# Kernel optimization log

Measured on AMD Instinct MI355X. Metric: run time of the kernel, lower is better.

The kernel has to match this reference:

```python
import jax, jax.numpy as jnp
import numpy as np

N_SAMPLES = 2 ** 16  # 65536


def sparse_softmax(x, axis=-1):
    # forward: one-hot at argmax (normalize=True -> value 1.0)
    # backward: softmax gradient (straight-through)
    sm = jax.nn.softmax(x, axis=axis)
    hard = jax.nn.one_hot(jnp.argmax(sm, axis=axis), x.shape[axis], dtype=x.dtype)
    return sm + jax.lax.stop_gradient(hard - sm)


def upsample_with_holes(x, desired_size):
    # strided zero-insertion: out[..., ::step] = x
    step = desired_size // x.shape[-1]
    out = jnp.zeros(x.shape[:-1] + (desired_size,), dtype=x.dtype)
    return out.at[..., ::step].set(x)


def fft_convolve(a, b):
    # circular-safe convolution: pad both to 2n, multiply spectra, keep first n
    n = a.shape[-1]
    pad_a = [(0, 0)] * (a.ndim - 1) + [(0, n)]
    pad_b = [(0, 0)] * (b.ndim - 1) + [(0, n)]
    spec = jnp.fft.rfft(jnp.pad(a, pad_a), axis=-1) * jnp.fft.rfft(jnp.pad(b, pad_b), axis=-1)
    return jnp.fft.irfft(spec, axis=-1)[..., :n]


def setup_inputs() -> dict:
    key = jax.random.key(0)
    k1, k2 = jax.random.split(key)
    events = jax.random.normal(k1, (8, 32, N_SAMPLES), dtype=jnp.float32)
    # nn.Parameter uniform_(-1, 1)
    pos = jax.random.uniform(k2, (1, 32, 1024), dtype=jnp.float32, minval=-1.0, maxval=1.0)
    return {"events": events, "pos": pos}


def reference(events, pos):
    p = sparse_softmax(pos, axis=-1)                 # (1, 32, 1024) one-hot
    p = upsample_with_holes(p, N_SAMPLES)            # (1, 32, 65536) sparse diracs
    return fft_convolve(events, p)                   # (8, 32, 65536)
```

## Files before the change

kernel.cpp:

```cpp
#include <hip/hip_runtime.h>

#define N_SAMPLES 65536
#define POS_LEN   1024
#define STEP      64
#define NCH       32
#define NB        8
#define ROW4      (N_SAMPLES / 4)

__global__ void argmax_kernel(const float* __restrict__ pos, int* __restrict__ delay) {
    const int c    = blockIdx.x;
    const int lane = threadIdx.x;
    const float* row = pos + c * POS_LEN;

    float best = -__builtin_inff();
    int   bidx = POS_LEN;
    for (int k = lane; k < POS_LEN; k += 64) {
        float v = row[k];
        if (v > best) { best = v; bidx = k; }
    }
    for (int off = 32; off > 0; off >>= 1) {
        float ov = __shfl_down(best, off, 64);
        int   oi = __shfl_down(bidx, off, 64);
        if (ov > best || (ov == best && oi < bidx)) { best = ov; bidx = oi; }
    }
    if (lane == 0) delay[c] = bidx * STEP;
}

__global__ void shift_kernel(const float4* __restrict__ in, float4* __restrict__ out,
                             const int* __restrict__ delay) {
    __shared__ int sdelay4[NCH];
    if (threadIdx.x < NCH) sdelay4[threadIdx.x] = delay[threadIdx.x] >> 2;
    __syncthreads();

    const int total  = NB * NCH * ROW4;
    const int stride = gridDim.x * blockDim.x;
    for (int i = blockIdx.x * blockDim.x + threadIdx.x; i < total; i += stride) {
        const int t4 = i & (ROW4 - 1);
        const int c  = (i >> 14) & (NCH - 1);
        const int d4 = sdelay4[c];
        float4 v;
        if (t4 >= d4) {
            v = in[i - d4];
        } else {
            v = make_float4(0.f, 0.f, 0.f, 0.f);
        }
        out[i] = v;
    }
}

extern "C" void kernel_launch(void* const* d_in, const int* in_sizes, int n_in,
                              void* d_out, int out_size, void* d_ws, size_t ws_size,
                              hipStream_t stream) {
    const float* events = (const float*)d_in[0];
    const float* pos    = (const float*)d_in[1];
    float*       out    = (float*)d_out;
    int*         delay  = (int*)d_ws;

    argmax_kernel<<<NCH, 64, 0, stream>>>(pos, delay);

    shift_kernel<<<2048, 256, 0, stream>>>((const float4*)events, (float4*)out, delay);
}
```

Baseline: 119.6 us.

## Fuse argmax into shift kernel with per-row segment blocks and nontemporal I/O

Merges the argmax and shift kernels into one launch. Each block recomputes its channel's argmax with a 256-thread reduction and then copies one segment of a row with a fixed unrolled loop, using nontemporal loads and stores. This removes a kernel launch, the workspace round trip and the dependency between the two kernels. In exchange, each of the 2048 blocks redundantly reads 4 KB of pos and performs a block reduction with two syncs before streaming.

Measured after the change: 118.9 us. Within noise of the previous version (-0.6%).

```diff
diff --git a/kernel.cpp b/kernel.cpp
--- a/kernel.cpp
+++ b/kernel.cpp
@@ -6,45 +6,64 @@
 #define NCH       32
 #define NB        8
 #define ROW4      (N_SAMPLES / 4)
+#define SEGS      8
+#define SEG4      (ROW4 / SEGS)
 
-__global__ void argmax_kernel(const float* __restrict__ pos, int* __restrict__ delay) {
-    const int c    = blockIdx.x;
-    const int lane = threadIdx.x;
-    const float* row = pos + c * POS_LEN;
+typedef float f32x4 __attribute__((ext_vector_type(4)));
 
-    float best = -__builtin_inff();
-    int   bidx = POS_LEN;
-    for (int k = lane; k < POS_LEN; k += 64) {
-        float v = row[k];
-        if (v > best) { best = v; bidx = k; }
+__global__ __launch_bounds__(256) void dirac_shift(const float* __restrict__ pos,
+                                                   const f32x4* __restrict__ in,
+                                                   f32x4* __restrict__ out) {
+    const int g   = blockIdx.x;
+    const int row = g >> 3;
+    const int seg = g & (SEGS - 1);
+    const int c   = row & (NCH - 1);
+    const int tid = threadIdx.x;
+
+    __shared__ float swv[4];
+    __shared__ int   swi[4];
+    __shared__ int   sd4;
+
+    {
+        const f32x4 v = ((const f32x4*)(pos + c * POS_LEN))[tid];
+        float best = v[0];
+        int   bidx = tid * 4;
+        #pragma unroll
+        for (int j = 1; j < 4; ++j) {
+            if (v[j] > best) { best = v[j]; bidx = tid * 4 + j; }
+        }
+        #pragma unroll
+        for (int off = 32; off > 0; off >>= 1) {
+            float ov = __shfl_down(best, off, 64);
+            int   oi = __shfl_down(bidx, off, 64);
+            if (ov > best || (ov == best && oi < bidx)) { best = ov; bidx = oi; }
+        }
+        const int lane = tid & 63, wave = tid >> 6;
+        if (lane == 0) { swv[wave] = best; swi[wave] = bidx; }
     }
-    for (int off = 32; off > 0; off >>= 1) {
-        float ov = __shfl_down(best, off, 64);
-        int   oi = __shfl_down(bidx, off, 64);
-        if (ov > best || (ov == best && oi < bidx)) { best = ov; bidx = oi; }
+    __syncthreads();
+    if (tid == 0) {
+        float best = swv[0];
+        int   bidx = swi[0];
+        #pragma unroll
+        for (int w = 1; w < 4; ++w) {
+            if (swv[w] > best || (swv[w] == best && swi[w] < bidx)) { best = swv[w]; bidx = swi[w]; }
+        }
+        sd4 = bidx * (STEP / 4);
     }
-    if (lane == 0) delay[c] = bidx * STEP;
-}
-
-__global__ void shift_kernel(const float4* __restrict__ in, float4* __restrict__ out,
-                             const int* __restrict__ delay) {
-    __shared__ int sdelay4[NCH];
-    if (threadIdx.x < NCH) sdelay4[threadIdx.x] = delay[threadIdx.x] >> 2;
     __syncthreads();
 
-    const int total  = NB * NCH * ROW4;
-    const int stride = gridDim.x * blockDim.x;
-    for (int i = blockIdx.x * blockDim.x + threadIdx.x; i < total; i += stride) {
-        const int t4 = i & (ROW4 - 1);
-        const int c  = (i >> 14) & (NCH - 1);
-        const int d4 = sdelay4[c];
-        float4 v;
-        if (t4 >= d4) {
-            v = in[i - d4];
-        } else {
-            v = make_float4(0.f, 0.f, 0.f, 0.f);
-        }
-        out[i] = v;
+    const int d4 = sd4;
+    const f32x4* inrow  = in  + (size_t)row * ROW4;
+    f32x4*       outrow = out + (size_t)row * ROW4;
+    const int base = seg * SEG4;
+
+    #pragma unroll
+    for (int k = 0; k < SEG4 / 256; ++k) {
+        const int t4 = base + k * 256 + tid;
+        f32x4 v = {0.f, 0.f, 0.f, 0.f};
+        if (t4 >= d4) v = __builtin_nontemporal_load(inrow + (t4 - d4));
+        __builtin_nontemporal_store(v, outrow + t4);
     }
 }
 
@@ -54,9 +73,6 @@
     const float* events = (const float*)d_in[0];
     const float* pos    = (const float*)d_in[1];
     float*       out    = (float*)d_out;
-    int*         delay  = (int*)d_ws;
 
-    argmax_kernel<<<NCH, 64, 0, stream>>>(pos, delay);
-
-    shift_kernel<<<2048, 256, 0, stream>>>((const float4*)events, (float4*)out, delay);
+    dirac_shift<<<NB * NCH * SEGS, 256, 0, stream>>>(pos, (const f32x4*)events, (f32x4*)out);
 }
```
